# Kernel tuning notes

Measured on AMD Instinct MI355X. Metric: run time of the kernel, lower is better.

Reference implementation:

```python
import jax, jax.numpy as jnp
import numpy as np

HIDDEN = 1024
HEADS = 16
HEAD_DIM = HIDDEN // HEADS
FF = 4 * HIDDEN
B, S = 2, 2048


def _linear_params(key, out_dim, in_dim):
    kw, kb = jax.random.split(key)
    bound = 1.0 / np.sqrt(in_dim)
    W = jax.random.uniform(kw, (out_dim, in_dim), jnp.float32, -bound, bound)
    b = jax.random.uniform(kb, (out_dim,), jnp.float32, -bound, bound)
    return W, b


def setup_inputs() -> dict:
    key = jax.random.key(0)
    ks = jax.random.split(key, 8)
    x = jax.random.normal(ks[0], (B, S, HIDDEN), jnp.float32)
    attention_mask = jnp.ones((B, S), jnp.float32)
    Wq, bq = _linear_params(ks[1], HIDDEN, HIDDEN)
    Wk, bk = _linear_params(ks[2], HIDDEN, HIDDEN)
    Wv, bv = _linear_params(ks[3], HIDDEN, HIDDEN)
    Wo, bo = _linear_params(ks[4], HIDDEN, HIDDEN)
    W1, b1 = _linear_params(ks[5], FF, HIDDEN)
    W2, b2 = _linear_params(ks[6], HIDDEN, FF)
    g1 = jnp.ones((HIDDEN,), jnp.float32); be1 = jnp.zeros((HIDDEN,), jnp.float32)
    g2 = jnp.ones((HIDDEN,), jnp.float32); be2 = jnp.zeros((HIDDEN,), jnp.float32)
    return dict(x=x, attention_mask=attention_mask,
                Wq=Wq, bq=bq, Wk=Wk, bk=bk, Wv=Wv, bv=bv, Wo=Wo, bo=bo,
                W1=W1, b1=b1, W2=W2, b2=b2,
                g1=g1, be1=be1, g2=g2, be2=be2)


def _layer_norm(x, g, b, eps=1e-5):
    mu = jnp.mean(x, axis=-1, keepdims=True)
    var = jnp.mean(jnp.square(x - mu), axis=-1, keepdims=True)
    return (x - mu) * jax.lax.rsqrt(var + eps) * g + b


def reference(x, attention_mask, Wq, bq, Wk, bk, Wv, bv, Wo, bo,
              W1, b1, W2, b2, g1, be1, g2, be2):
    # Dropout is identity (eval mode / deterministic reference).
    residual = x
    h = _layer_norm(x, g1, be1)
    # [B,S,H] -> [B,nH,S,dh]
    def heads(t):
        return t.reshape(B, S, HEADS, HEAD_DIM).transpose(0, 2, 1, 3)
    q = heads(h @ Wq.T + bq)
    k = heads(h @ Wk.T + bk)
    v = heads(h @ Wv.T + bv)
    scores = jnp.einsum('bhqd,bhkd->bhqk', q, k) / np.sqrt(HEAD_DIM).astype(np.float32)
    scores = scores + (attention_mask[:, None, None, :] - 1.0) * 10000.0
    attn = jax.nn.softmax(scores, axis=-1)
    ctx = jnp.einsum('bhqk,bhkd->bhqd', attn, v)
    ctx = ctx.transpose(0, 2, 1, 3).reshape(B, S, HIDDEN)
    attn_out = ctx @ Wo.T + bo
    x = residual + attn_out
    residual = x
    h = _layer_norm(x, g2, be2)
    h = jax.nn.gelu(h @ W1.T + b1, approximate=False)
    h = h @ W2.T + b2
    return residual + h
```

## Files before the change

### kernel.cpp

```cpp
#include <hip/hip_runtime.h>
#include <hip/hip_bf16.h>
#include <math.h>

typedef __bf16 bf16;
typedef __bf16 bf16x2 __attribute__((ext_vector_type(2)));
typedef __bf16 bf16x4v __attribute__((ext_vector_type(4)));
typedef __bf16 bf16x8 __attribute__((ext_vector_type(8)));
typedef float  f32x4  __attribute__((ext_vector_type(4)));
typedef unsigned u32x4 __attribute__((ext_vector_type(4)));
typedef unsigned u32x2 __attribute__((ext_vector_type(2)));

#define HIDDEN 1024
#define TOKENS 4096
#define FFDIM  4096
#define SEQ    2048
#define NHEAD  16

#define LOG2E 1.44269504088896340736f

__device__ __forceinline__ void async_copy16(bf16* lds, const bf16* g)
{
    __builtin_amdgcn_global_load_lds(
        (__attribute__((address_space(1))) void*)g,
        (__attribute__((address_space(3))) void*)lds,
        16, 0, 0);
}

__device__ __forceinline__ unsigned pack2(float lo, float hi)
{
    bf16x2 t; t[0] = (bf16)lo; t[1] = (bf16)hi;
    return __builtin_bit_cast(unsigned, t);
}

__device__ __forceinline__ void pl32swap(unsigned& a, unsigned& b)
{
    u32x2 r = __builtin_amdgcn_permlane32_swap(a, b, false, false);
    a = r.x; b = r.y;
}

__device__ __forceinline__ float gelu_fast(float v)
{
    float x = fabsf(v) * 0.70710678118654752f;
    float t = __builtin_amdgcn_rcpf(1.0f + 0.3275911f * x);
    float p = t * (0.254829592f + t * (-0.284496736f + t * (1.421413741f + t * (-1.453152027f + t * 1.061405429f))));
    float e = __builtin_amdgcn_exp2f(-x * x * LOG2E);
    float erfv = 1.0f - p * e;
    erfv = (v < 0.0f) ? -erfv : erfv;
    return 0.5f * v * (1.0f + erfv);
}

__global__ __launch_bounds__(256) void cvt_all_kernel(const float* __restrict__ wq,
    const float* __restrict__ wk, const float* __restrict__ wv, const float* __restrict__ wo,
    const float* __restrict__ w1, const float* __restrict__ w2, bf16* __restrict__ out)
{
    size_t i = ((size_t)blockIdx.x * 256 + threadIdx.x) * 4;
    int sel = (int)(i >> 20);
    const float* src;
    size_t off;
    if (sel < 4) { src = (sel == 0) ? wq : (sel == 1) ? wk : (sel == 2) ? wv : wo; off = i & ((1u << 20) - 1); }
    else if (sel < 8) { src = w1; off = i - ((size_t)4 << 20); }
    else              { src = w2; off = i - ((size_t)8 << 20); }
    float4 v = *(const float4*)&src[off];
    bf16x4v o = { (bf16)v.x, (bf16)v.y, (bf16)v.z, (bf16)v.w };
    *(bf16x4v*)&out[i] = o;
}

__global__ __launch_bounds__(256) void concat_bias_kernel(const float* __restrict__ bq,
    const float* __restrict__ bk, const float* __restrict__ bv, float* __restrict__ o)
{
    int i = blockIdx.x * 256 + threadIdx.x;
    float v = (i < 1024) ? bq[i] : (i < 2048 ? bk[i - 1024] : bv[i - 2048]);
    o[i] = v;
}

__global__ __launch_bounds__(256) void ln_kernel(const float* __restrict__ in,
    const float* __restrict__ g, const float* __restrict__ be, bf16* __restrict__ out)
{
    int row = blockIdx.x;
    int tid = threadIdx.x;
    const float* x = in + (size_t)row * HIDDEN;
    int i0 = tid * 4;
    float4 v = *(const float4*)&x[i0];
    float s  = v.x + v.y + v.z + v.w;
    float s2 = v.x*v.x + v.y*v.y + v.z*v.z + v.w*v.w;
    #pragma unroll
    for (int off = 32; off > 0; off >>= 1) { s += __shfl_xor(s, off); s2 += __shfl_xor(s2, off); }
    __shared__ float red[2][4];
    int wave = tid >> 6;
    if ((tid & 63) == 0) { red[0][wave] = s; red[1][wave] = s2; }
    __syncthreads();
    float ts  = red[0][0] + red[0][1] + red[0][2] + red[0][3];
    float ts2 = red[1][0] + red[1][1] + red[1][2] + red[1][3];
    float mu   = ts  * (1.0f / HIDDEN);
    float var  = ts2 * (1.0f / HIDDEN) - mu * mu;
    float rstd = rsqrtf(var + 1e-5f);
    float4 gg = *(const float4*)&g[i0];
    float4 bb = *(const float4*)&be[i0];
    bf16x4v o;
    o[0] = (bf16)((v.x - mu) * rstd * gg.x + bb.x);
    o[1] = (bf16)((v.y - mu) * rstd * gg.y + bb.y);
    o[2] = (bf16)((v.z - mu) * rstd * gg.z + bb.z);
    o[3] = (bf16)((v.w - mu) * rstd * gg.w + bb.w);
    *(bf16x4v*)&out[(size_t)row * HIDDEN + i0] = o;
}

template<int BM, int EPI, typename OT>
__global__ __launch_bounds__(256) void gemm_bt(const bf16* __restrict__ A, const bf16* __restrict__ Bt,
    const float* __restrict__ bias, const float* __restrict__ res, OT* __restrict__ C,
    int M, int N, int K)
{
    constexpr int MT = BM / 32;
    __shared__ bf16 As[2][BM * 64];
    __shared__ bf16 Bs[2][128 * 64];
    int tid  = threadIdx.x;
    int wave = tid >> 6, lane = tid & 63;
    int lm = lane & 15, quad = lane >> 4;
    int m0 = blockIdx.x * BM, n0 = blockIdx.y * 128;
    int wm = (wave >> 1) * (MT * 16), wn = (wave & 1) * 64;
    int r8 = lane >> 3, c8 = lane & 7;
    int gsw = (c8 ^ (r8 & 7)) * 8;
    auto stage = [&](int buf, int k0) {
        #pragma unroll
        for (int ch = wave; ch < BM / 8; ch += 4)
            async_copy16(&As[buf][ch * 512], &A[(size_t)(m0 + ch * 8 + r8) * K + k0 + gsw]);
        #pragma unroll
        for (int ch = wave; ch < 16; ch += 4)
            async_copy16(&Bs[buf][ch * 512], &Bt[(size_t)(n0 + ch * 8 + r8) * K + k0 + gsw]);
    };
    f32x4 acc[MT][4] = {};
    stage(0, 0);
    int nk = K >> 6;
    for (int t = 0; t < nk; t++) {
        __syncthreads();
        if (t + 1 < nk) stage((t + 1) & 1, (t + 1) * 64);
        const bf16* as = As[t & 1];
        const bf16* bs = Bs[t & 1];
        bf16x8 af[MT][2], bfr[4][2];
        #pragma unroll
        for (int ks = 0; ks < 2; ks++) {
            int co = ((ks * 4 + quad) ^ (lm & 7)) * 8;
            #pragma unroll
            for (int t2 = 0; t2 < MT; t2++) af[t2][ks]  = *(const bf16x8*)&as[(wm + t2 * 16 + lm) * 64 + co];
            #pragma unroll
            for (int t2 = 0; t2 < 4; t2++)  bfr[t2][ks] = *(const bf16x8*)&bs[(wn + t2 * 16 + lm) * 64 + co];
        }
        #pragma unroll
        for (int mt = 0; mt < MT; mt++)
            #pragma unroll
            for (int nt = 0; nt < 4; nt++)
                #pragma unroll
                for (int ks = 0; ks < 2; ks++)
                    acc[mt][nt] = __builtin_amdgcn_mfma_f32_16x16x32_bf16(af[mt][ks], bfr[nt][ks], acc[mt][nt], 0, 0, 0);
    }
    #pragma unroll
    for (int mt = 0; mt < MT; mt++) {
        #pragma unroll
        for (int nt = 0; nt < 4; nt++) {
            int col = n0 + wn + nt * 16 + lm;
            float bv = bias[col];
            #pragma unroll
            for (int r = 0; r < 4; r++) {
                int row = m0 + wm + mt * 16 + quad * 4 + r;
                float vv = acc[mt][nt][r] + bv;
                if (EPI == 1) vv = gelu_fast(vv);
                if (EPI == 2) vv += res[(size_t)row * N + col];
                C[(size_t)row * N + col] = (OT)vv;
            }
        }
    }
}

__global__ __launch_bounds__(256) void gemm_qkv(const bf16* __restrict__ A, const bf16* __restrict__ W,
    const float* __restrict__ bias, bf16* __restrict__ qb, bf16* __restrict__ kb, bf16* __restrict__ vt)
{
    constexpr int K = HIDDEN;
    __shared__ bf16 As[2][128 * 64];
    __shared__ bf16 Bs[2][128 * 64];
    int tid  = threadIdx.x;
    int wave = tid >> 6, lane = tid & 63;
    int lm = lane & 15, quad = lane >> 4;
    int m0 = blockIdx.x * 128, n0 = blockIdx.y * 128;
    int wm = (wave >> 1) * 64, wn = (wave & 1) * 64;
    int r8 = lane >> 3, c8 = lane & 7;
    int gsw = (c8 ^ (r8 & 7)) * 8;
    auto stage = [&](int buf, int k0) {
        #pragma unroll
        for (int ch = wave; ch < 16; ch += 4) {
            async_copy16(&As[buf][ch * 512], &A[(size_t)(m0 + ch * 8 + r8) * K + k0 + gsw]);
            async_copy16(&Bs[buf][ch * 512], &W[(size_t)(n0 + ch * 8 + r8) * K + k0 + gsw]);
        }
    };
    f32x4 acc[4][4] = {};
    stage(0, 0);
    constexpr int nk = K >> 6;
    for (int t = 0; t < nk; t++) {
        __syncthreads();
        if (t + 1 < nk) stage((t + 1) & 1, (t + 1) * 64);
        const bf16* as = As[t & 1];
        const bf16* bs = Bs[t & 1];
        bf16x8 af[4][2], bfr[4][2];
        #pragma unroll
        for (int ks = 0; ks < 2; ks++) {
            int co = ((ks * 4 + quad) ^ (lm & 7)) * 8;
            #pragma unroll
            for (int t2 = 0; t2 < 4; t2++) {
                af[t2][ks]  = *(const bf16x8*)&as[(wm + t2 * 16 + lm) * 64 + co];
                bfr[t2][ks] = *(const bf16x8*)&bs[(wn + t2 * 16 + lm) * 64 + co];
            }
        }
        #pragma unroll
        for (int mt = 0; mt < 4; mt++)
            #pragma unroll
            for (int nt = 0; nt < 4; nt++)
                #pragma unroll
                for (int ks = 0; ks < 2; ks++)
                    acc[mt][nt] = __builtin_amdgcn_mfma_f32_16x16x32_bf16(af[mt][ks], bfr[nt][ks], acc[mt][nt], 0, 0, 0);
    }
    int region = n0 >> 10;
    #pragma unroll
    for (int mt = 0; mt < 4; mt++) {
        #pragma unroll
        for (int nt = 0; nt < 4; nt++) {
            int col = n0 + wn + nt * 16 + lm;
            float bv = bias[col];
            int cl = col & 1023;
            #pragma unroll
            for (int r = 0; r < 4; r++) {
                int row = m0 + wm + mt * 16 + quad * 4 + r;
                float vv = acc[mt][nt][r] + bv;
                if (region == 0)      qb[(size_t)row * HIDDEN + cl] = (bf16)vv;
                else if (region == 1) kb[(size_t)row * HIDDEN + cl] = (bf16)vv;
                else {
                    int h = cl >> 6, d = cl & 63;
                    int b = row >> 11, s = row & 2047;
                    vt[(((size_t)(b * NHEAD + h)) * 64 + d) * SEQ + s] = (bf16)vv;
                }
            }
        }
    }
}

__global__ __launch_bounds__(512, 4) void attn_kernel(const bf16* __restrict__ Q, const bf16* __restrict__ K,
    const bf16* __restrict__ Vt, const float* __restrict__ mask, bf16* __restrict__ O)
{
    __shared__ bf16 smem[32768];
    int tid = threadIdx.x, wave = tid >> 6, lane = tid & 63;
    int lm = lane & 15, quad = lane >> 4;
    int pair = wave >> 1, h = wave & 1;
    int bh = blockIdx.y, b = bh >> 4;
    int q0 = blockIdx.x * 128 + pair * 32;
    const size_t base  = ((size_t)b * SEQ) * HIDDEN + (bh & 15) * 64;
    const size_t vbase = (size_t)bh * 64 * SEQ;
    int srow8 = lane >> 3, spos = lane & 7;
    bf16x8 qf[2][2];
    #pragma unroll
    for (int qt = 0; qt < 2; qt++)
        #pragma unroll
        for (int ks = 0; ks < 2; ks++)
            qf[qt][ks] = *(const bf16x8*)&Q[base + (size_t)(q0 + qt * 16 + lm) * HIDDEN + ks * 32 + quad * 8];
    bf16x8 onesf;
    #pragma unroll
    for (int i = 0; i < 8; i++) onesf[i] = (bf16)1.0f;
    f32x4 o[2][4] = {};
    f32x4 lacc[2] = {};
    const float c0 = 0.125f * LOG2E;
    const float cmk = 10000.0f * LOG2E;
    const float coff = -(cmk + 16.0f);
    int r = wave * 8 + srow8;
    int gc = spos ^ (r & 7);
    auto stage = [&](int gbuf, int ktg) {
        #pragma unroll
        for (int s = 0; s < 2; s++) {
            bf16* kd = smem + ((gbuf << 1) + s) * 4096;
            bf16* vd = smem + 16384 + ((gbuf << 1) + s) * 4096;
            int kt = ktg + s * 64;
            async_copy16(kd + wave * 512, &K [base  + (size_t)(kt + r) * HIDDEN + gc * 8]);
            async_copy16(vd + wave * 512, &Vt[vbase + (size_t)r * SEQ + kt + gc * 8]);
        }
    };
    stage(0, 0);
    int kh = h * 32;
    bool qodd = (quad & 1);
    for (int gi = 0; gi < SEQ / 128; gi++) {
        __syncthreads();
        if (gi + 1 < SEQ / 128) stage((gi + 1) & 1, (gi + 1) * 128);
        #pragma unroll
        for (int sub = 0; sub < 2; sub++) {
            const bf16* ksb = smem + (((gi & 1) << 1) + sub) * 4096;
            const bf16* vsb = smem + 16384 + (((gi & 1) << 1) + sub) * 4096;
            int kt = gi * 128 + sub * 64;
            bf16x8 kf[2][2];
            #pragma unroll
            for (int nt = 0; nt < 2; nt++)
                #pragma unroll
                for (int ks = 0; ks < 2; ks++)
                    kf[nt][ks] = *(const bf16x8*)&ksb[(kh + nt * 16 + lm) * 64 + (((ks * 4 + quad) ^ (lm & 7)) * 8)];
            f32x4 st[2][2] = {};
            #pragma unroll
            for (int qt = 0; qt < 2; qt++)
                #pragma unroll
                for (int nt = 0; nt < 2; nt++)
                    #pragma unroll
                    for (int ks = 0; ks < 2; ks++)
                        st[qt][nt] = __builtin_amdgcn_mfma_f32_16x16x32_bf16(kf[nt][ks], qf[qt][ks], st[qt][nt], 0, 0, 0);
            float madd[2][4];
            #pragma unroll
            for (int nt = 0; nt < 2; nt++) {
                float4 mv = *(const float4*)&mask[b * SEQ + kt + kh + nt * 16 + quad * 4];
                madd[nt][0] = mv.x * cmk + coff; madd[nt][1] = mv.y * cmk + coff;
                madd[nt][2] = mv.z * cmk + coff; madd[nt][3] = mv.w * cmk + coff;
            }
            bf16x8 af[2];
            #pragma unroll
            for (int qt = 0; qt < 2; qt++) {
                unsigned w[2][2];
                #pragma unroll
                for (int nt = 0; nt < 2; nt++) {
                    float p0 = __builtin_amdgcn_exp2f(st[qt][nt][0] * c0 + madd[nt][0]);
                    float p1 = __builtin_amdgcn_exp2f(st[qt][nt][1] * c0 + madd[nt][1]);
                    float p2 = __builtin_amdgcn_exp2f(st[qt][nt][2] * c0 + madd[nt][2]);
                    float p3 = __builtin_amdgcn_exp2f(st[qt][nt][3] * c0 + madd[nt][3]);
                    w[nt][0] = pack2(p0, p1);
                    w[nt][1] = pack2(p2, p3);
                }
                unsigned A0 = w[0][0], B0 = w[1][0];
                unsigned A1 = w[0][1], B1 = w[1][1];
                pl32swap(A0, B0);
                pl32swap(A1, B1);
                unsigned F0 = __shfl_xor(A0, 16), G0 = __shfl_xor(B0, 16);
                unsigned F1 = __shfl_xor(A1, 16), G1 = __shfl_xor(B1, 16);
                u32x4 uu;
                uu.x = qodd ? G0 : A0;
                uu.y = qodd ? G1 : A1;
                uu.z = qodd ? B0 : F0;
                uu.w = qodd ? B1 : F1;
                af[qt] = __builtin_bit_cast(bf16x8, uu);
                lacc[qt] = __builtin_amdgcn_mfma_f32_16x16x32_bf16(af[qt], onesf, lacc[qt], 0, 0, 0);
            }
            #pragma unroll
            for (int dt = 0; dt < 4; dt++) {
                bf16x8 vf = *(const bf16x8*)&vsb[(dt * 16 + lm) * 64 + (((4 * h + quad) ^ (lm & 7)) * 8)];
                #pragma unroll
                for (int qt = 0; qt < 2; qt++)
                    o[qt][dt] = __builtin_amdgcn_mfma_f32_16x16x32_bf16(af[qt], vf, o[qt][dt], 0, 0, 0);
            }
        }
    }
    __syncthreads();
    float* scratch = (float*)smem;
    float* s = scratch + ((size_t)pair * 64 + lane) * 20;
    if (h == 1) {
        #pragma unroll
        for (int dt = 0; dt < 4; dt++) *(f32x4*)&s[dt * 4] = o[0][dt];
        *(f32x4*)&s[16] = lacc[0];
    }
    __syncthreads();
    if (h == 0) {
        f32x4 pl = *(const f32x4*)&s[16];
        #pragma unroll
        for (int rr = 0; rr < 4; rr++) {
            float inv = 1.0f / (lacc[0][rr] + pl[rr]);
            #pragma unroll
            for (int dt = 0; dt < 4; dt++) {
                float val = (o[0][dt][rr] + s[dt * 4 + rr]) * inv;
                O[base + (size_t)(q0 + quad * 4 + rr) * HIDDEN + dt * 16 + lm] = (bf16)val;
            }
        }
    }
    __syncthreads();
    if (h == 0) {
        #pragma unroll
        for (int dt = 0; dt < 4; dt++) *(f32x4*)&s[dt * 4] = o[1][dt];
        *(f32x4*)&s[16] = lacc[1];
    }
    __syncthreads();
    if (h == 1) {
        f32x4 pl = *(const f32x4*)&s[16];
        #pragma unroll
        for (int rr = 0; rr < 4; rr++) {
            float inv = 1.0f / (lacc[1][rr] + pl[rr]);
            #pragma unroll
            for (int dt = 0; dt < 4; dt++) {
                float val = (o[1][dt][rr] + s[dt * 4 + rr]) * inv;
                O[base + (size_t)(q0 + 16 + quad * 4 + rr) * HIDDEN + dt * 16 + lm] = (bf16)val;
            }
        }
    }
}

extern "C" void kernel_launch(void* const* d_in, const int* in_sizes, int n_in,
                              void* d_out, int out_size, void* d_ws, size_t ws_size,
                              hipStream_t stream)
{
    (void)in_sizes; (void)n_in; (void)out_size; (void)ws_size;
    const float* x    = (const float*)d_in[0];
    const float* mask = (const float*)d_in[1];
    const float* Wq   = (const float*)d_in[2];
    const float* bq   = (const float*)d_in[3];
    const float* Wk   = (const float*)d_in[4];
    const float* bk   = (const float*)d_in[5];
    const float* Wv   = (const float*)d_in[6];
    const float* bv   = (const float*)d_in[7];
    const float* Wo   = (const float*)d_in[8];
    const float* bo   = (const float*)d_in[9];
    const float* W1   = (const float*)d_in[10];
    const float* b1   = (const float*)d_in[11];
    const float* W2   = (const float*)d_in[12];
    const float* b2   = (const float*)d_in[13];
    const float* g1   = (const float*)d_in[14];
    const float* be1  = (const float*)d_in[15];
    const float* g2   = (const float*)d_in[16];
    const float* be2  = (const float*)d_in[17];
    float* out = (float*)d_out;

    const size_t M1 = 1024u * 1024u;
    bf16* ws    = (bf16*)d_ws;
    bf16* Wqkv_b = ws;
    bf16* Wo_b  = ws + 3 * M1;
    bf16* W1_b  = ws + 4 * M1;
    bf16* W2_b  = ws + 8 * M1;
    bf16* qb    = ws + 12 * M1;
    bf16* kb    = ws + 16 * M1;
    bf16* vt    = ws + 20 * M1;
    bf16* cx    = ws + 24 * M1;
    bf16* h     = ws + 28 * M1;
    bf16* ffb   = ws + 12 * M1;
    float* biasqkv = (float*)(ws + 24 * M1);

    cvt_all_kernel<<<dim3(12288), 256, 0, stream>>>(Wq, Wk, Wv, Wo, W1, W2, Wqkv_b);
    concat_bias_kernel<<<dim3(12), 256, 0, stream>>>(bq, bk, bv, biasqkv);

    ln_kernel<<<dim3(TOKENS), 256, 0, stream>>>(x, g1, be1, h);
    gemm_qkv<<<dim3(32, 24), 256, 0, stream>>>(h, Wqkv_b, biasqkv, qb, kb, vt);
    attn_kernel<<<dim3(SEQ / 128, 32), 512, 0, stream>>>(qb, kb, vt, mask, cx);
    gemm_bt<64, 2, float><<<dim3(64, 8), 256, 0, stream>>>(cx, Wo_b, bo, x, out, TOKENS, HIDDEN, HIDDEN);
    ln_kernel<<<dim3(TOKENS), 256, 0, stream>>>(out, g2, be2, h);
    gemm_bt<128, 1, bf16><<<dim3(32, 32), 256, 0, stream>>>(h, W1_b, b1, nullptr, ffb, TOKENS, FFDIM, HIDDEN);
    gemm_bt<64, 2, float><<<dim3(64, 8), 256, 0, stream>>>(ffb, W2_b, b2, out, out, TOKENS, HIDDEN, FFDIM);
}
```

Before: 355.7 us.

## Use explicit vmcnt waits and split barriers to overlap prefetch in GEMM/attention

Replaces __syncthreads in the GEMM and attention main loops with a barrier, an issue of the next stage's async LDS copies, and a partial s_waitcnt vmcnt(N). The wait covers only the current stage's loads, followed by a second barrier, so the prefetch stays in flight during compute instead of being fully drained. It also stages the attention mask into LDS once per block instead of reading it from global memory every tile. The risk is that the hand-computed vmcnt counts must exactly match the number of loads issued per wave, otherwise compute could read incomplete data. The added second barrier per iteration is extra synchronisation cost.

```diff
diff --git a/kernel.cpp b/kernel.cpp
--- a/kernel.cpp
+++ b/kernel.cpp
@@ -24,6 +24,14 @@
         (__attribute__((address_space(1))) void*)g,
         (__attribute__((address_space(3))) void*)lds,
         16, 0, 0);
+}
+
+template<int N> __device__ __forceinline__ void waitv()
+{
+    if constexpr (N == 0)      asm volatile("s_waitcnt vmcnt(0)" ::: "memory");
+    else if constexpr (N == 4) asm volatile("s_waitcnt vmcnt(4)" ::: "memory");
+    else if constexpr (N == 6) asm volatile("s_waitcnt vmcnt(6)" ::: "memory");
+    else if constexpr (N == 8) asm volatile("s_waitcnt vmcnt(8)" ::: "memory");
 }
 
 __device__ __forceinline__ unsigned pack2(float lo, float hi)
@@ -110,6 +118,7 @@
     int M, int N, int K)
 {
     constexpr int MT = BM / 32;
+    constexpr int CP = BM / 32 + 4;
     __shared__ bf16 As[2][BM * 64];
     __shared__ bf16 Bs[2][128 * 64];
     int tid  = threadIdx.x;
@@ -131,8 +140,14 @@
     stage(0, 0);
     int nk = K >> 6;
     for (int t = 0; t < nk; t++) {
-        __syncthreads();
-        if (t + 1 < nk) stage((t + 1) & 1, (t + 1) * 64);
+        __builtin_amdgcn_sched_barrier(0);
+        __builtin_amdgcn_s_barrier();
+        bool pre = (t + 1 < nk);
+        if (pre) stage((t + 1) & 1, (t + 1) * 64);
+        if (pre) waitv<CP>(); else waitv<0>();
+        __builtin_amdgcn_sched_barrier(0);
+        __builtin_amdgcn_s_barrier();
+        __builtin_amdgcn_sched_barrier(0);
         const bf16* as = As[t & 1];
         const bf16* bs = Bs[t & 1];
         bf16x8 af[MT][2], bfr[4][2];
@@ -194,8 +209,14 @@
     stage(0, 0);
     constexpr int nk = K >> 6;
     for (int t = 0; t < nk; t++) {
-        __syncthreads();
-        if (t + 1 < nk) stage((t + 1) & 1, (t + 1) * 64);
+        __builtin_amdgcn_sched_barrier(0);
+        __builtin_amdgcn_s_barrier();
+        bool pre = (t + 1 < nk);
+        if (pre) stage((t + 1) & 1, (t + 1) * 64);
+        if (pre) waitv<8>(); else waitv<0>();
+        __builtin_amdgcn_sched_barrier(0);
+        __builtin_amdgcn_s_barrier();
+        __builtin_amdgcn_sched_barrier(0);
         const bf16* as = As[t & 1];
         const bf16* bs = Bs[t & 1];
         bf16x8 af[4][2], bfr[4][2];
@@ -244,6 +265,7 @@
     const bf16* __restrict__ Vt, const float* __restrict__ mask, bf16* __restrict__ O)
 {
     __shared__ bf16 smem[32768];
+    __shared__ float maskLds[SEQ];
     int tid = threadIdx.x, wave = tid >> 6, lane = tid & 63;
     int lm = lane & 15, quad = lane >> 4;
     int pair = wave >> 1, h = wave & 1;
@@ -252,6 +274,7 @@
     const size_t base  = ((size_t)b * SEQ) * HIDDEN + (bh & 15) * 64;
     const size_t vbase = (size_t)bh * 64 * SEQ;
     int srow8 = lane >> 3, spos = lane & 7;
+    ((float4*)maskLds)[tid] = ((const float4*)(mask + (size_t)b * SEQ))[tid];
     bf16x8 qf[2][2];
     #pragma unroll
     for (int qt = 0; qt < 2; qt++)
@@ -282,8 +305,14 @@
     int kh = h * 32;
     bool qodd = (quad & 1);
     for (int gi = 0; gi < SEQ / 128; gi++) {
-        __syncthreads();
-        if (gi + 1 < SEQ / 128) stage((gi + 1) & 1, (gi + 1) * 128);
+        __builtin_amdgcn_sched_barrier(0);
+        __builtin_amdgcn_s_barrier();
+        bool pre = gi + 1 < SEQ / 128;
+        if (pre) stage((gi + 1) & 1, (gi + 1) * 128);
+        if (pre) waitv<4>(); else waitv<0>();
+        __builtin_amdgcn_sched_barrier(0);
+        __builtin_amdgcn_s_barrier();
+        __builtin_amdgcn_sched_barrier(0);
         #pragma unroll
         for (int sub = 0; sub < 2; sub++) {
             const bf16* ksb = smem + (((gi & 1) << 1) + sub) * 4096;
@@ -306,7 +335,7 @@
             float madd[2][4];
             #pragma unroll
             for (int nt = 0; nt < 2; nt++) {
-                float4 mv = *(const float4*)&mask[b * SEQ + kt + kh + nt * 16 + quad * 4];
+                float4 mv = *(const float4*)&maskLds[kt + kh + nt * 16 + quad * 4];
                 madd[nt][0] = mv.x * cmk + coff; madd[nt][1] = mv.y * cmk + coff;
                 madd[nt][2] = mv.z * cmk + coff; madd[nt][3] = mv.w * cmk + coff;
             }
```

Result: no change. 351.1 us (-1.3%).
